# Kernel tuning notes

Measured on AMD Instinct MI355X. Metric: run time of the kernel, lower is better.

## Reference

```python
import jax, jax.numpy as jnp
import numpy as np
from jax import lax

B, IN_CH, OUT_CH, K, STYLE_DIM, H, W = 4, 512, 512, 3, 512, 64, 64


def setup_inputs() -> dict:
    key = jax.random.key(0)
    ks = jax.random.split(key, 6)
    x = jax.random.normal(ks[0], (B, B * IN_CH, H, W), dtype=jnp.float32)
    style = jax.random.normal(ks[1], (B, STYLE_DIM), dtype=jnp.float32)
    # learned params
    weight = jax.random.normal(ks[2], (1, OUT_CH, IN_CH, K, K), dtype=jnp.float32)
    demod = jnp.ones((1, OUT_CH, 1, 1), dtype=jnp.float32)
    # nn.Linear(style_dim, in_channels): kaiming-uniform-ish init approximated
    lim = 1.0 / np.sqrt(STYLE_DIM)
    mod_w = jax.random.uniform(ks[3], (IN_CH, STYLE_DIM), minval=-lim, maxval=lim, dtype=jnp.float32)
    mod_b = jax.random.uniform(ks[4], (IN_CH,), minval=-lim, maxval=lim, dtype=jnp.float32)
    return {"x": x, "style": style, "weight": weight, "demod": demod, "mod_w": mod_w, "mod_b": mod_b}


def reference(x, style, weight, demod, mod_w, mod_b):
    b = x.shape[0]
    out_ch, in_ch, k = weight.shape[1], weight.shape[2], weight.shape[3]
    # style modulation: Linear(style) -> (B, in_ch) -> (B,1,in_ch,1,1)
    s = style @ mod_w.T + mod_b
    w = weight * s[:, None, :, None, None]          # (B, out, in, k, k)
    # demod (1,out,1,1) broadcasts against trailing (in,k,k) axes -> needs out==in (as in torch)
    w = w * demod
    w = w.reshape(b * out_ch, in_ch, k, k)           # OIHW grouped kernel
    pad = k // 2
    out = lax.conv_general_dilated(
        x, w,
        window_strides=(1, 1),
        padding=[(pad, pad), (pad, pad)],
        dimension_numbers=("NCHW", "OIHW", "NCHW"),
        feature_group_count=b,
    )
    return out  # (B, B*out_ch, H, W)
```

## Files before the change

kernel.cpp:

```cpp
#include <hip/hip_runtime.h>

typedef __attribute__((ext_vector_type(4))) float f32x4;
typedef __attribute__((ext_vector_type(8))) short bf16x8;
typedef unsigned long long u64;
typedef unsigned short u16;
typedef unsigned int u32;

static __device__ __forceinline__ u16 f2bf(float f) {
    u32 u = __float_as_uint(f);
    u += 0x7fffu + ((u >> 16) & 1u);
    return (u16)(u >> 16);
}

__global__ void k_style(const float* __restrict__ style, const float* __restrict__ mod_w,
                        const float* __restrict__ mod_b, float* __restrict__ s_ws) {
    int t = blockIdx.x * 256 + threadIdx.x;
    int g = t >> 9, ic = t & 511;
    const f32x4* st = (const f32x4*)(style + (g << 9));
    const f32x4* mw = (const f32x4*)(mod_w + (ic << 9));
    float acc = 0.f;
#pragma unroll 4
    for (int d = 0; d < 128; ++d) {
        f32x4 a = st[d], b = mw[d];
        acc += a[0]*b[0] + a[1]*b[1] + a[2]*b[2] + a[3]*b[3];
    }
    s_ws[t] = acc + mod_b[ic];
}

__global__ void k_wmod(const float* __restrict__ weight, const float* __restrict__ demod,
                       const float* __restrict__ s_ws, short* __restrict__ wmod) {
    int t = blockIdx.x * 256 + threadIdx.x;
    int lane = t & 63; int r = t >> 6;
    int m = r & 3; r >>= 2;
    int ch = r & 15; r >>= 4;
    int wr = r & 1; r >>= 1;
    int ocb = r & 3; r >>= 2;
    int g = r & 3;
    int oc  = ocb*128 + wr*64 + m*16 + (lane & 15);
    int ic0 = ch*32 + (lane >> 4)*8;
    const float* wp = weight + (size_t)(oc*512 + ic0)*9;
    float sv[8];
#pragma unroll
    for (int e = 0; e < 8; ++e) sv[e] = s_ws[(g << 9) + ic0 + e] * demod[ic0 + e];
    short* base = wmod + ((size_t)((g*4 + ocb)*2 + wr)) * 294912 + ((size_t)m << 9) + (lane << 3);
#pragma unroll
    for (int tp = 0; tp < 9; ++tp) {
        bf16x8 pk;
#pragma unroll
        for (int e = 0; e < 8; ++e) pk[e] = (short)f2bf(wp[e*9 + tp] * sv[e]);
        *(bf16x8*)&base[(size_t)(ch*9 + tp) << 11] = pk;
    }
}

__global__ __launch_bounds__(256) void k_xcast(const float* __restrict__ x,
                                               short* __restrict__ xb) {
    __shared__ short Ls[64 * 520];
    const int tid = threadIdx.x;
    const int y = blockIdx.x, g = blockIdx.y, nb = blockIdx.z;
    const float* src = x + (((size_t)(nb * 2048 + (g << 9))) << 12) + (y << 6);
#pragma unroll
    for (int it = 0; it < 32; ++it) {
        int j = it * 256 + tid;
        int ic = j >> 4, p4 = j & 15;
        f32x4 v = *(const f32x4*)(src + ((size_t)ic << 12) + (p4 << 2));
        int kk = (ic >> 3) & 3;
        int fb = (ic >> 5) * 32 + (ic & 7);
#pragma unroll
        for (int c = 0; c < 4; ++c) {
            int px = (p4 << 2) + c;
            int k = kk ^ ((px >> 1) & 3);
            Ls[px * 520 + fb + k * 8] = (short)f2bf(v[c]);
        }
    }
    __syncthreads();
    short* dstb = xb + ((size_t)((nb * 4 + g) * 64 + y) << 15);
#pragma unroll
    for (int it = 0; it < 16; ++it) {
        int j = it * 256 + tid;
        int ch = j >> 8, px = (j >> 2) & 63, k = j & 3;
        *(bf16x8*)&dstb[(size_t)j << 3] = *(const bf16x8*)&Ls[px * 520 + ch * 32 + k * 8];
    }
}

__global__ __launch_bounds__(256, 4) void k_conv(const short* __restrict__ xb,
                                                 const short* __restrict__ wmod,
                                                 float* __restrict__ out) {
    __shared__ __align__(16) short Xs[2 * 8448];

    const int tid  = threadIdx.x;
    const int lane = tid & 63;
    const int wv   = tid >> 6;
    const int wr   = wv >> 1, wc = wv & 1;
    const int l15  = lane & 15;
    const int l4   = lane >> 4;
    const int ocb  = blockIdx.x >> 5, rowb = blockIdx.x & 31;
    const int g    = blockIdx.y, nb = blockIdx.z;
    const int y0   = rowb << 1;

    const short* xbg = xb + ((size_t)((nb * 4 + g) * 64) << 15);
    const short* wg  = wmod + ((size_t)((g * 4 + ocb) * 2 + wr)) * 294912;
    float* outg = out + (((size_t)(nb * 2048 + (g << 9) + ocb * 128)) << 12) + (rowb << 7);

    const int gy = y0 - 1 + wv;
    const bool srow = (gy >= 0 && gy <= 63);
    const short* xsrc = xbg + ((size_t)(srow ? gy : 0) << 15) + (lane << 3);
    short* xdst0 = Xs + ((wv * 66 + 1) << 5);

    const short* wp = wg + (lane << 3);

    for (int i = tid; i < 4224; i += 256) ((u64*)Xs)[i] = 0ull;

    f32x4 acc[4][4];
#pragma unroll
    for (int m = 0; m < 4; ++m)
#pragma unroll
        for (int nn = 0; nn < 4; ++nn) acc[m][nn] = (f32x4){0.f, 0.f, 0.f, 0.f};

    __syncthreads();

    if (srow) {
#pragma unroll
        for (int q = 0; q < 4; ++q)
            __builtin_amdgcn_global_load_lds(
                (const __attribute__((address_space(1))) void*)(xsrc + (q << 9)),
                (__attribute__((address_space(3))) void*)(xdst0 + (q << 9)), 16, 0, 0);
    }
    __builtin_amdgcn_sched_barrier(0);
    bf16x8 na0 = *(const bf16x8*)(wp);
    bf16x8 na1 = *(const bf16x8*)(wp + 512);
    bf16x8 na2 = *(const bf16x8*)(wp + 1024);
    bf16x8 na3 = *(const bf16x8*)(wp + 1536);
    wp += 2048;

#pragma unroll 1
    for (int ch = 0; ch < 16; ++ch) {
        asm volatile("s_waitcnt vmcnt(4)" ::: "memory");
        __builtin_amdgcn_s_barrier();
        __builtin_amdgcn_sched_barrier(0);
        if (ch < 15 && srow) {
            const short* s = xsrc + ((size_t)(ch + 1) << 11);
            short* d = xdst0 + (((ch + 1) & 1) ? 8448 : 0);
#pragma unroll
            for (int q = 0; q < 4; ++q)
                __builtin_amdgcn_global_load_lds(
                    (const __attribute__((address_space(1))) void*)(s + (q << 9)),
                    (__attribute__((address_space(3))) void*)(d + (q << 9)), 16, 0, 0);
        }
        __builtin_amdgcn_sched_barrier(0);
        const int bb = (ch & 1) * 8448;

        int pB[3];
#pragma unroll
        for (int d = 0; d < 3; ++d) {
            const int dx = d - 1;
            pB[d] = bb + ((wc * 66 + 1 + dx + l15) << 5)
                  + ((l4 ^ (((l15 + dx) >> 1) & 3)) << 3);
        }

#pragma unroll
        for (int tap = 0; tap < 9; ++tap) {
            bf16x8 ca0 = na0, ca1 = na1, ca2 = na2, ca3 = na3;
            na0 = *(const bf16x8*)(wp);
            na1 = *(const bf16x8*)(wp + 512);
            na2 = *(const bf16x8*)(wp + 1024);
            na3 = *(const bf16x8*)(wp + 1536);
            wp += 2048;

            const int p0 = pB[tap % 3] + (tap / 3) * 2112;
            bf16x8 b0 = *(const bf16x8*)&Xs[p0];
            bf16x8 b1 = *(const bf16x8*)&Xs[p0 + 512];
            bf16x8 b2 = *(const bf16x8*)&Xs[p0 + 1024];
            bf16x8 b3 = *(const bf16x8*)&Xs[p0 + 1536];

            __builtin_amdgcn_s_setprio(1);
            acc[0][0] = __builtin_amdgcn_mfma_f32_16x16x32_bf16(ca0, b0, acc[0][0], 0, 0, 0);
            acc[1][0] = __builtin_amdgcn_mfma_f32_16x16x32_bf16(ca1, b0, acc[1][0], 0, 0, 0);
            acc[2][0] = __builtin_amdgcn_mfma_f32_16x16x32_bf16(ca2, b0, acc[2][0], 0, 0, 0);
            acc[3][0] = __builtin_amdgcn_mfma_f32_16x16x32_bf16(ca3, b0, acc[3][0], 0, 0, 0);
            acc[0][1] = __builtin_amdgcn_mfma_f32_16x16x32_bf16(ca0, b1, acc[0][1], 0, 0, 0);
            acc[1][1] = __builtin_amdgcn_mfma_f32_16x16x32_bf16(ca1, b1, acc[1][1], 0, 0, 0);
            acc[2][1] = __builtin_amdgcn_mfma_f32_16x16x32_bf16(ca2, b1, acc[2][1], 0, 0, 0);
            acc[3][1] = __builtin_amdgcn_mfma_f32_16x16x32_bf16(ca3, b1, acc[3][1], 0, 0, 0);
            acc[0][2] = __builtin_amdgcn_mfma_f32_16x16x32_bf16(ca0, b2, acc[0][2], 0, 0, 0);
            acc[1][2] = __builtin_amdgcn_mfma_f32_16x16x32_bf16(ca1, b2, acc[1][2], 0, 0, 0);
            acc[2][2] = __builtin_amdgcn_mfma_f32_16x16x32_bf16(ca2, b2, acc[2][2], 0, 0, 0);
            acc[3][2] = __builtin_amdgcn_mfma_f32_16x16x32_bf16(ca3, b2, acc[3][2], 0, 0, 0);
            acc[0][3] = __builtin_amdgcn_mfma_f32_16x16x32_bf16(ca0, b3, acc[0][3], 0, 0, 0);
            acc[1][3] = __builtin_amdgcn_mfma_f32_16x16x32_bf16(ca1, b3, acc[1][3], 0, 0, 0);
            acc[2][3] = __builtin_amdgcn_mfma_f32_16x16x32_bf16(ca2, b3, acc[2][3], 0, 0, 0);
            acc[3][3] = __builtin_amdgcn_mfma_f32_16x16x32_bf16(ca3, b3, acc[3][3], 0, 0, 0);
            __builtin_amdgcn_s_setprio(0);
        }
    }

#pragma unroll
    for (int m = 0; m < 4; ++m)
#pragma unroll
        for (int nn = 0; nn < 4; ++nn) {
            const int oc = (wr << 6) + (m << 4) + (l4 << 2);
            const int p  = (wc << 6) + (nn << 4) + l15;
            float* dst = outg + ((size_t)oc << 12) + p;
#pragma unroll
            for (int r = 0; r < 4; ++r) dst[(size_t)r << 12] = acc[m][nn][r];
        }
}

extern "C" void kernel_launch(void* const* d_in, const int* in_sizes, int n_in,
                              void* d_out, int out_size, void* d_ws, size_t ws_size,
                              hipStream_t stream) {
    const float* x      = (const float*)d_in[0];
    const float* style  = (const float*)d_in[1];
    const float* weight = (const float*)d_in[2];
    const float* demod  = (const float*)d_in[3];
    const float* mod_w  = (const float*)d_in[4];
    const float* mod_b  = (const float*)d_in[5];
    float* out = (float*)d_out;

    float* s_ws = (float*)d_ws;
    short* wmod = (short*)((char*)d_ws + 8192);
    short* xbuf = (short*)((char*)d_ws + 8192 + 18874368);

    hipLaunchKernelGGL(k_style, dim3(8), dim3(256), 0, stream, style, mod_w, mod_b, s_ws);
    hipLaunchKernelGGL(k_wmod, dim3(512), dim3(256), 0, stream, weight, demod, s_ws, wmod);
    hipLaunchKernelGGL(k_xcast, dim3(64, 4, 4), dim3(256), 0, stream, x, xbuf);
    hipLaunchKernelGGL(k_conv, dim3(128, 4, 4), dim3(256), 0, stream, xbuf, wmod, out);
}
```

Measured before the change: 310.3 us.

## Enlarge conv block to four output rows with eight waves

The conv kernel now computes four output rows per block instead of two, using 512 threads (8 waves) and a six-row LDS input slab. Each wave issues three async global-to-LDS loads so the halo rows are spread across the block. This lowers the fraction of halo rows loaded per output row and lets more waves share the same weight stream. The launch bound of 512 threads with 4 blocks per CU caps the register budget tightly, so the 64-float accumulator may spill. The larger LDS footprint per block may also reduce how many blocks fit on a CU.

```diff
diff --git a/kernel.cpp b/kernel.cpp
--- a/kernel.cpp
+++ b/kernel.cpp
@@ -82,33 +82,39 @@
     }
 }
 
-__global__ __launch_bounds__(256, 4) void k_conv(const short* __restrict__ xb,
+__global__ __launch_bounds__(512, 4) void k_conv(const short* __restrict__ xb,
                                                  const short* __restrict__ wmod,
                                                  float* __restrict__ out) {
-    __shared__ __align__(16) short Xs[2 * 8448];
+    __shared__ __align__(16) short Xs[2 * 12672];
 
     const int tid  = threadIdx.x;
     const int lane = tid & 63;
     const int wv   = tid >> 6;
-    const int wr   = wv >> 1, wc = wv & 1;
+    const int wr   = wv >> 2, wc = wv & 3;
     const int l15  = lane & 15;
     const int l4   = lane >> 4;
-    const int ocb  = blockIdx.x >> 5, rowb = blockIdx.x & 31;
+    const int ocb  = blockIdx.x >> 4, rowb = blockIdx.x & 15;
     const int g    = blockIdx.y, nb = blockIdx.z;
-    const int y0   = rowb << 1;
+    const int y0   = rowb << 2;
 
     const short* xbg = xb + ((size_t)((nb * 4 + g) * 64) << 15);
     const short* wg  = wmod + ((size_t)((g * 4 + ocb) * 2 + wr)) * 294912;
-    float* outg = out + (((size_t)(nb * 2048 + (g << 9) + ocb * 128)) << 12) + (rowb << 7);
-
-    const int gy = y0 - 1 + wv;
-    const bool srow = (gy >= 0 && gy <= 63);
-    const short* xsrc = xbg + ((size_t)(srow ? gy : 0) << 15) + (lane << 3);
-    short* xdst0 = Xs + ((wv * 66 + 1) << 5);
+    float* outg = out + (((size_t)(nb * 2048 + (g << 9) + ocb * 128)) << 12) + (rowb << 8);
+
+    const short* sB[3]; int dO[3]; bool ok[3];
+#pragma unroll
+    for (int i = 0; i < 3; ++i) {
+        const int id = wv * 3 + i;
+        const int row = id >> 2, q = id & 3;
+        const int gy = y0 - 1 + row;
+        ok[i] = (gy >= 0 && gy <= 63);
+        sB[i] = xbg + ((size_t)(ok[i] ? gy : 0) << 15) + (q << 9) + (lane << 3);
+        dO[i] = (row * 66 + 1 + (q << 4)) << 5;
+    }
 
     const short* wp = wg + (lane << 3);
 
-    for (int i = tid; i < 4224; i += 256) ((u64*)Xs)[i] = 0ull;
+    for (int i = tid; i < 6336; i += 512) ((u64*)Xs)[i] = 0ull;
 
     f32x4 acc[4][4];
 #pragma unroll
@@ -118,13 +124,12 @@
 
     __syncthreads();
 
-    if (srow) {
-#pragma unroll
-        for (int q = 0; q < 4; ++q)
+#pragma unroll
+    for (int i = 0; i < 3; ++i)
+        if (ok[i])
             __builtin_amdgcn_global_load_lds(
-                (const __attribute__((address_space(1))) void*)(xsrc + (q << 9)),
-                (__attribute__((address_space(3))) void*)(xdst0 + (q << 9)), 16, 0, 0);
-    }
+                (const __attribute__((address_space(1))) void*)(sB[i]),
+                (__attribute__((address_space(3))) void*)(Xs + dO[i]), 16, 0, 0);
     __builtin_amdgcn_sched_barrier(0);
     bf16x8 na0 = *(const bf16x8*)(wp);
     bf16x8 na1 = *(const bf16x8*)(wp + 512);
@@ -137,17 +142,18 @@
         asm volatile("s_waitcnt vmcnt(4)" ::: "memory");
         __builtin_amdgcn_s_barrier();
         __builtin_amdgcn_sched_barrier(0);
-        if (ch < 15 && srow) {
-            const short* s = xsrc + ((size_t)(ch + 1) << 11);
-            short* d = xdst0 + (((ch + 1) & 1) ? 8448 : 0);
-#pragma unroll
-            for (int q = 0; q < 4; ++q)
-                __builtin_amdgcn_global_load_lds(
-                    (const __attribute__((address_space(1))) void*)(s + (q << 9)),
-                    (__attribute__((address_space(3))) void*)(d + (q << 9)), 16, 0, 0);
+        if (ch < 15) {
+            const int chN = ch + 1;
+            short* dbase = Xs + ((chN & 1) ? 12672 : 0);
+#pragma unroll
+            for (int i = 0; i < 3; ++i)
+                if (ok[i])
+                    __builtin_amdgcn_global_load_lds(
+                        (const __attribute__((address_space(1))) void*)(sB[i] + ((size_t)chN << 11)),
+                        (__attribute__((address_space(3))) void*)(dbase + dO[i]), 16, 0, 0);
         }
         __builtin_amdgcn_sched_barrier(0);
-        const int bb = (ch & 1) * 8448;
+        const int bb = (ch & 1) * 12672;
 
         int pB[3];
 #pragma unroll
@@ -223,5 +229,5 @@
     hipLaunchKernelGGL(k_style, dim3(8), dim3(256), 0, stream, style, mod_w, mod_b, s_ws);
     hipLaunchKernelGGL(k_wmod, dim3(512), dim3(256), 0, stream, weight, demod, s_ws, wmod);
     hipLaunchKernelGGL(k_xcast, dim3(64, 4, 4), dim3(256), 0, stream, x, xbuf);
-    hipLaunchKernelGGL(k_conv, dim3(128, 4, 4), dim3(256), 0, stream, xbuf, wmod, out);
-}
+    hipLaunchKernelGGL(k_conv, dim3(64, 4, 4), dim3(512), 0, stream, xbuf, wmod, out);
+}
```

Measured after the change: 315.3 us. Within noise of the previous version (+1.6%).
